# Kernel tuning notes

Hardware: AMD Instinct MI355X
Metric: run time of the kernel (lower is better)

## Reference

```python
import jax, jax.numpy as jnp
import numpy as np

# 4-neighbor cross stencil deltas from CONNECTION_FLAGS_3x3_small
DELTAS = ((-1, 0), (0, -1), (0, 1), (1, 0))


def setup_inputs() -> dict:
    key = jax.random.key(0)
    k1, k2, k3 = jax.random.split(key, 3)
    B, G, C, H, W = 4, 8, 32, 128, 128
    patchs = jax.random.normal(k1, (B, G, C, H, W), dtype=jnp.float32)
    edge_weights = jax.random.uniform(k2, (B, G, 4, H, W), dtype=jnp.float32)
    node_degree = jax.random.uniform(k3, (B, G, H, W), dtype=jnp.float32)
    return {"patchs": patchs, "edge_weights": edge_weights, "node_degree": node_degree}


def _gather_neighbors(x):
    # x: [B, GC, H, W] -> [B, GC, 4, H, W] with replicate padding (torch 'replicate' == jnp 'edge')
    B, GC, H, W = x.shape
    xp = jnp.pad(x, ((0, 0), (0, 0), (1, 1), (1, 1)), mode='edge')
    nbrs = [xp[:, :, 1 + dh:1 + dh + H, 1 + dw:1 + dw + W] for dh, dw in DELTAS]
    return jnp.stack(nbrs, axis=2)


def reference(patchs, edge_weights, node_degree):
    # patchs: [B, G, C, H, W]; edge_weights: [B, G, 4, H, W]; node_degree unused in forward
    B, G, C, H, W = patchs.shape
    x = patchs.reshape(B, G * C, H, W)
    nbrs = _gather_neighbors(x).reshape(B, G, C, 4, H, W)
    Wx = jnp.einsum('bgcehw,bgehw->bgchw', nbrs, edge_weights)
    return patchs - Wx
```

## Files before the change

kernel.cpp:

```cpp
#include <hip/hip_runtime.h>


#define GLR_HW 16384

typedef float fvec4 __attribute__((ext_vector_type(4)));

__global__ __launch_bounds__(256, 4) void glr_fwd_kernel(
    const float* __restrict__ patchs,
    const float* __restrict__ ew,
    float* __restrict__ out)
{
    __shared__ float4 sw[2048];

    const int t  = threadIdx.x;
    const int w4 = t & 31;
    const int cl = t >> 5;

    const int bg     = blockIdx.x >> 5;
    const int strip  = (blockIdx.x >> 2) & 7;
    const int cgroup = blockIdx.x & 3;

    const int r0 = strip << 4;
    const int w  = w4 << 2;

    const int plane = (bg << 5) + (cgroup << 3) + cl;
    const float* __restrict__ P = patchs + (size_t)plane * GLR_HW + w;
    float*       __restrict__ O = out    + (size_t)plane * GLR_HW + w;

    float4 reg[18];
    #pragma unroll
    for (int i = 0; i < 18; ++i) {
        int r = r0 + i - 1;
        r = (r < 0) ? 0 : (r > 127 ? 127 : r);
        reg[i] = *(const float4*)(P + (r << 7));
    }

    {
        const float* __restrict__ EW = ew + (size_t)bg * 4 * GLR_HW;
        #pragma unroll
        for (int k = 0; k < 8; ++k) {
            const int j  = t + (k << 8);
            const int e  = j >> 9;
            const int i  = (j >> 5) & 15;
            const int wq = j & 31;
            sw[j] = *(const float4*)(EW + e * GLR_HW + ((r0 + i) << 7) + (wq << 2));
        }
    }
    __syncthreads();

    const bool atL = (w4 == 0);
    const bool atR = (w4 == 31);

    #pragma unroll
    for (int i = 0; i < 16; ++i) {
        const float4 up  = reg[i];
        const float4 cur = reg[i + 1];
        const float4 dn  = reg[i + 2];

        const int si = (i << 5) + w4;
        const float4 e0 = sw[si];
        const float4 e1 = sw[512 + si];
        const float4 e2 = sw[1024 + si];
        const float4 e3 = sw[1536 + si];

        float lf = __shfl_up(cur.w, 1);
        float rg = __shfl_down(cur.x, 1);
        if (atL) lf = cur.x;
        if (atR) rg = cur.w;

        fvec4 o;
        o.x = cur.x - (up.x * e0.x + lf    * e1.x + cur.y * e2.x + dn.x * e3.x);
        o.y = cur.y - (up.y * e0.y + cur.x * e1.y + cur.z * e2.y + dn.y * e3.y);
        o.z = cur.z - (up.z * e0.z + cur.y * e1.z + cur.w * e2.z + dn.z * e3.z);
        o.w = cur.w - (up.w * e0.w + cur.z * e1.w + rg    * e2.w + dn.w * e3.w);

        *(fvec4*)(O + ((r0 + i) << 7)) = o;
    }
}

extern "C" void kernel_launch(void* const* d_in, const int* in_sizes, int n_in,
                              void* d_out, int out_size, void* d_ws, size_t ws_size,
                              hipStream_t stream) {
    const float* patchs = (const float*)d_in[0];
    const float* ew     = (const float*)d_in[1];
    float* out = (float*)d_out;

    glr_fwd_kernel<<<1024, 256, 0, stream>>>(patchs, ew, out);
}
```

Baseline: 124.3 us.

## Double block size so each edge-weight tile is shared by sixteen channels

Blocks grow to 512 threads covering 16 channel planes, so the edge-weight tile for a strip is loaded once per 16 channels instead of once per 8. That halves redundant edge-weight global reads. The weight loads are also issued into registers before the patch loads, which overlaps them with the stencil loads. Block indices are remapped so adjacent blocks cover different batch-groups. This leaves 512 blocks, which may reduce scheduling flexibility, and the 512-thread launch bound with 18 float4 registers per thread may raise register pressure.

```diff
diff --git a/kernel.cpp b/kernel.cpp
--- a/kernel.cpp
+++ b/kernel.cpp
@@ -5,7 +5,7 @@
 
 typedef float fvec4 __attribute__((ext_vector_type(4)));
 
-__global__ __launch_bounds__(256, 4) void glr_fwd_kernel(
+__global__ __launch_bounds__(512, 4) void glr_fwd_kernel(
     const float* __restrict__ patchs,
     const float* __restrict__ ew,
     float* __restrict__ out)
@@ -14,18 +14,28 @@
 
     const int t  = threadIdx.x;
     const int w4 = t & 31;
-    const int cl = t >> 5;
+    const int ch = t >> 5;
 
-    const int bg     = blockIdx.x >> 5;
-    const int strip  = (blockIdx.x >> 2) & 7;
-    const int cgroup = blockIdx.x & 3;
+    const int b     = blockIdx.x;
+    const int q     = b >> 3;
+    const int bg    = (b & 7) + ((q >> 4) << 3);
+    const int rr    = q & 15;
+    const int strip = rr >> 1;
+    const int hf    = rr & 1;
 
     const int r0 = strip << 4;
     const int w  = w4 << 2;
 
-    const int plane = (bg << 5) + (cgroup << 3) + cl;
+    const int plane = (bg << 5) + (hf << 4) + ch;
     const float* __restrict__ P = patchs + (size_t)plane * GLR_HW + w;
     float*       __restrict__ O = out    + (size_t)plane * GLR_HW + w;
+
+    const float* __restrict__ EW =
+        ew + (size_t)bg * 4 * GLR_HW + ((r0 + ch) << 7) + w;
+    float4 wreg[4];
+    #pragma unroll
+    for (int k = 0; k < 4; ++k)
+        wreg[k] = *(const float4*)(EW + k * GLR_HW);
 
     float4 reg[18];
     #pragma unroll
@@ -35,17 +45,9 @@
         reg[i] = *(const float4*)(P + (r << 7));
     }
 
-    {
-        const float* __restrict__ EW = ew + (size_t)bg * 4 * GLR_HW;
-        #pragma unroll
-        for (int k = 0; k < 8; ++k) {
-            const int j  = t + (k << 8);
-            const int e  = j >> 9;
-            const int i  = (j >> 5) & 15;
-            const int wq = j & 31;
-            sw[j] = *(const float4*)(EW + e * GLR_HW + ((r0 + i) << 7) + (wq << 2));
-        }
-    }
+    #pragma unroll
+    for (int k = 0; k < 4; ++k)
+        sw[t + (k << 9)] = wreg[k];
     __syncthreads();
 
     const bool atL = (w4 == 0);
@@ -85,5 +87,5 @@
     const float* ew     = (const float*)d_in[1];
     float* out = (float*)d_out;
 
-    glr_fwd_kernel<<<1024, 256, 0, stream>>>(patchs, ew, out);
+    glr_fwd_kernel<<<512, 512, 0, stream>>>(patchs, ew, out);
 }
```

New measurement: 122.6 us. Within noise of the previous version (-1.3%).
